# Optimization experiments

Measured on AMD Instinct MI355X. Metric: run time of the kernel, lower is better.

## Reference

```python
import jax, jax.numpy as jnp
import numpy as np

C = 256
NUM_GROUPS = 32
EPS = 1e-5


def group_norm(x, gamma, beta):
    # x: [B, C, H, W]; normalize within each of NUM_GROUPS channel groups
    B, Cc, H, W = x.shape
    xg = x.reshape(B, NUM_GROUPS, Cc // NUM_GROUPS, H, W)
    mean = xg.mean(axis=(2, 3, 4), keepdims=True)
    var = xg.var(axis=(2, 3, 4), keepdims=True)
    xg = (xg - mean) * jax.lax.rsqrt(var + EPS)
    x = xg.reshape(B, Cc, H, W)
    return x * gamma[None, :, None, None] + beta[None, :, None, None]


def conv1x1(x, w, b):
    # w: [C_out, C_in], b: [C_out]; equivalent to nn.Conv2d(k=1)
    return jnp.einsum('oc,bchw->bohw', w, x) + b[None, :, None, None]


def setup_inputs() -> dict:
    key = jax.random.key(0)
    ks = jax.random.split(key, 12)
    B, H, W = 8, 64, 64
    x = jax.random.normal(ks[0], (B, C, H, W), dtype=jnp.float32)
    temb = jax.random.normal(ks[1], (B, 512), dtype=jnp.float32)
    s = 1.0 / np.sqrt(C)  # kaiming-uniform-ish scale for 1x1 conv
    def wmat(k):
        return jax.random.uniform(k, (C, C), dtype=jnp.float32, minval=-s, maxval=s)
    def bvec(k):
        return jax.random.uniform(k, (C,), dtype=jnp.float32, minval=-s, maxval=s)
    return {
        'x': x, 'temb': temb,
        'gn_w': jnp.ones((C,), jnp.float32), 'gn_b': jnp.zeros((C,), jnp.float32),
        'wq': wmat(ks[2]), 'bq': bvec(ks[3]),
        'wk': wmat(ks[4]), 'bk': bvec(ks[5]),
        'wv': wmat(ks[6]), 'bv': bvec(ks[7]),
        'wp': wmat(ks[8]), 'bp': bvec(ks[9]),
    }


def reference(x, temb, gn_w, gn_b, wq, bq, wk, bk, wv, bv, wp, bp):
    B, Cc, H, W = x.shape
    h = group_norm(x, gn_w, gn_b)
    q = conv1x1(h, wq, bq)
    k = conv1x1(h, wk, bk)
    v = conv1x1(h, wv, bv)
    # full self-attention over spatial positions: scores [B, H, W, H, W]
    scale = Cc ** (-0.5)
    w = jnp.einsum('bchw,bcij->bhwij', q, k) * scale
    w = jax.nn.softmax(w.reshape(B, H, W, H * W), axis=-1).reshape(B, H, W, H, W)
    h = jnp.einsum('bhwij,bcij->bchw', w, v)
    h = conv1x1(h, wp, bp)
    return (x + h, temb)
```

## Files before the change

kernel.cpp:

```cpp
#include <hip/hip_runtime.h>
#include <hip/hip_bf16.h>

#define B_ 8
#define C_ 256
#define S_ 4096
#define G_ 32
#define GC_ 8
#define EPS_ 1e-5f

typedef __attribute__((ext_vector_type(4))) float f32x4;
typedef __attribute__((ext_vector_type(8))) short bf16x8;
typedef __attribute__((ext_vector_type(4))) short bf16x4;
typedef __attribute__((ext_vector_type(4))) unsigned int u32x4;
typedef __attribute__((ext_vector_type(2))) unsigned int u32x2;

#define DI __device__ __forceinline__

DI unsigned short f2bf(float f) {
    union { float f; unsigned u; } v; v.f = f;
    unsigned r = v.u + 0x7fffu + ((v.u >> 16) & 1u);
    return (unsigned short)(r >> 16);
}

DI unsigned cvt_pk_bf16(float lo, float hi) {
    unsigned r;
    asm("v_cvt_pk_bf16_f32 %0, %1, %2" : "=v"(r) : "v"(lo), "v"(hi));
    return r;
}

DI unsigned cvt_pk_fp8(float lo, float hi) {
    unsigned r;
    asm("v_cvt_pk_fp8_f32 %0, %1, %2" : "=v"(r) : "v"(lo), "v"(hi));
    return r;
}

DI f32x4 mfma_fp8(u32x2 a, u32x2 b, f32x4 c) {
    union { u32x2 u; long l; } ua, ub;
    ua.u = a; ub.u = b;
    return __builtin_amdgcn_mfma_f32_16x16x32_fp8_fp8(ua.l, ub.l, c, 0, 0, 0);
}

__global__ __launch_bounds__(256) void k_gn_stats(const float* __restrict__ x,
                                                  float* __restrict__ stats) {
    int bg = blockIdx.x;
    const float4* xp = (const float4*)(x + (size_t)bg * (GC_ * S_));
    float s = 0.f, ss = 0.f;
    for (int i = threadIdx.x; i < GC_ * S_ / 4; i += 256) {
        float4 v = xp[i];
        s  += v.x + v.y + v.z + v.w;
        ss += v.x * v.x + v.y * v.y + v.z * v.z + v.w * v.w;
    }
    #pragma unroll
    for (int off = 32; off; off >>= 1) { s += __shfl_down(s, off); ss += __shfl_down(ss, off); }
    __shared__ float rs[4], rss[4];
    int w = threadIdx.x >> 6;
    if ((threadIdx.x & 63) == 0) { rs[w] = s; rss[w] = ss; }
    __syncthreads();
    if (threadIdx.x == 0) {
        float S1 = rs[0] + rs[1] + rs[2] + rs[3];
        float S2 = rss[0] + rss[1] + rss[2] + rss[3];
        float inv = 1.f / (GC_ * S_);
        float mean = S1 * inv;
        float var = S2 * inv - mean * mean;
        stats[bg * 2] = mean;
        stats[bg * 2 + 1] = rsqrtf(var + EPS_);
    }
}

__global__ __launch_bounds__(256) void k_gn_apply(const float* __restrict__ x,
                                                  const float* __restrict__ stats,
                                                  const float* __restrict__ gw,
                                                  const float* __restrict__ gb,
                                                  unsigned short* __restrict__ h) {
    int b = blockIdx.x >> 6;
    int s0 = (blockIdx.x & 63) * 64;
    __shared__ unsigned short tile[64 * 256];
    const float* xb = x + (size_t)b * C_ * S_;
    for (int id = threadIdx.x; id < 256 * 16; id += 256) {
        int c = id >> 4, s4 = id & 15;
        float4 v = *(const float4*)(xb + (size_t)c * S_ + s0 + s4 * 4);
        float mean = stats[(b * G_ + (c >> 3)) * 2];
        float rstd = stats[(b * G_ + (c >> 3)) * 2 + 1];
        float ga = gw[c], be = gb[c];
        float vv[4] = {v.x, v.y, v.z, v.w};
        #pragma unroll
        for (int i = 0; i < 4; i++) {
            int srow = s4 * 4 + i;
            unsigned byte = srow * 512u + c * 2u;
            byte ^= ((srow & 7u) << 4);
            *(unsigned short*)((char*)tile + byte) = f2bf((vv[i] - mean) * rstd * ga + be);
        }
    }
    __syncthreads();
    unsigned short* hb = h + (size_t)b * S_ * C_;
    for (int id = threadIdx.x; id < 2048; id += 256) {
        int srow = id >> 5, ck = id & 31;
        unsigned byte = srow * 512u + ck * 16u;
        byte ^= ((srow & 7u) << 4);
        u32x4 v = *(u32x4*)((char*)tile + byte);
        *(u32x4*)(hb + (size_t)(s0 + srow) * C_ + ck * 8) = v;
    }
}

__global__ __launch_bounds__(256) void k_wcvt(const float* __restrict__ wq, const float* __restrict__ wk,
                                              const float* __restrict__ wv, const float* __restrict__ wp,
                                              unsigned short* __restrict__ wbf) {
    int t = blockIdx.x * 256 + threadIdx.x;
    int mat = t >> 13;
    int idx = (t & 8191) * 8;
    const float* src = mat == 0 ? wq : mat == 1 ? wk : mat == 2 ? wv : wp;
    float4 a = *(const float4*)(src + idx);
    float4 c = *(const float4*)(src + idx + 4);
    unsigned short tmp[8] = {f2bf(a.x), f2bf(a.y), f2bf(a.z), f2bf(a.w),
                             f2bf(c.x), f2bf(c.y), f2bf(c.z), f2bf(c.w)};
    *(u32x4*)(wbf + mat * 65536 + idx) = *(u32x4*)tmp;
}

__global__ __launch_bounds__(256) void k_qkv(const unsigned short* __restrict__ wbf,
                                             const float* __restrict__ bq,
                                             const float* __restrict__ bk,
                                             const float* __restrict__ bv,
                                             const unsigned short* __restrict__ h,
                                             unsigned char* __restrict__ q8,
                                             unsigned char* __restrict__ k8,
                                             unsigned short* __restrict__ v_cs) {
    int mode = blockIdx.x >> 9;
    int inner = blockIdx.x & 511;
    int b = inner & 7;
    int rest = inner >> 3;
    int m0 = (rest & 1) * 128;
    int n0 = (rest >> 1) * 128;
    const unsigned short* W = wbf + mode * 65536;
    const float* bias = mode == 0 ? bq : (mode == 1 ? bk : bv);

    __shared__ unsigned short Alds[128 * 64];
    __shared__ unsigned short Blds[128 * 64];
    int tid = threadIdx.x;
    int lane = tid & 63, wv = tid >> 6;
    int wm = (wv >> 1) * 64, wn = (wv & 1) * 64;
    int lr = lane & 15, lg = lane >> 4;
    f32x4 acc[4][4] = {};
    const unsigned short* Bb = h + (size_t)b * S_ * C_;

    for (int k0 = 0; k0 < 256; k0 += 64) {
        __syncthreads();
        #pragma unroll
        for (int i = 0; i < 4; i++) {
            int id = tid + i * 256;
            int row = id >> 3, ck = id & 7;
            u32x4 v = *(const u32x4*)(W + (size_t)(m0 + row) * C_ + k0 + ck * 8);
            unsigned byte = row * 128u + ck * 16u;
            byte ^= ((row & 7u) << 4);
            *(u32x4*)((char*)Alds + byte) = v;
        }
        #pragma unroll
        for (int i = 0; i < 4; i++) {
            int id = tid + i * 256;
            int row = id >> 3, ck = id & 7;
            u32x4 v = *(const u32x4*)(Bb + (size_t)(n0 + row) * C_ + k0 + ck * 8);
            unsigned byte = row * 128u + ck * 16u;
            byte ^= ((row & 7u) << 4);
            *(u32x4*)((char*)Blds + byte) = v;
        }
        __syncthreads();
        #pragma unroll
        for (int ks = 0; ks < 2; ks++) {
            bf16x8 af[4], bf[4];
            #pragma unroll
            for (int mf = 0; mf < 4; mf++) {
                int m = wm + mf * 16 + lr;
                unsigned byte = m * 128u + ks * 64u + lg * 16u;
                byte ^= ((m & 7u) << 4);
                af[mf] = *(bf16x8*)((char*)Alds + byte);
            }
            #pragma unroll
            for (int nf = 0; nf < 4; nf++) {
                int n = wn + nf * 16 + lr;
                unsigned byte = n * 128u + ks * 64u + lg * 16u;
                byte ^= ((n & 7u) << 4);
                bf[nf] = *(bf16x8*)((char*)Blds + byte);
            }
            #pragma unroll
            for (int mf = 0; mf < 4; mf++)
                #pragma unroll
                for (int nf = 0; nf < 4; nf++)
                    acc[mf][nf] = __builtin_amdgcn_mfma_f32_16x16x32_bf16(af[mf], bf[nf], acc[mf][nf], 0, 0, 0);
        }
    }

    if (mode < 2) {
        unsigned char* ob = (mode == 0 ? q8 : k8) + (size_t)b * S_ * C_;
        #pragma unroll
        for (int mf = 0; mf < 4; mf++)
            #pragma unroll
            for (int nf = 0; nf < 4; nf++) {
                int cbase = m0 + wm + mf * 16 + lg * 4;
                int srow = n0 + wn + nf * 16 + lr;
                float v0 = acc[mf][nf][0] + bias[cbase + 0];
                float v1 = acc[mf][nf][1] + bias[cbase + 1];
                float v2 = acc[mf][nf][2] + bias[cbase + 2];
                float v3 = acc[mf][nf][3] + bias[cbase + 3];
                unsigned lo = cvt_pk_fp8(v0, v1);
                unsigned hi = cvt_pk_fp8(v2, v3);
                *(unsigned*)(ob + (size_t)srow * C_ + cbase) = (lo & 0xffffu) | (hi << 16);
            }
    } else {
        unsigned short* ob = v_cs + (size_t)b * C_ * S_;
        #pragma unroll
        for (int mf = 0; mf < 4; mf++)
            #pragma unroll
            for (int nf = 0; nf < 4; nf++)
                #pragma unroll
                for (int r = 0; r < 4; r++) {
                    int c = m0 + wm + mf * 16 + lg * 4 + r;
                    int s = n0 + wn + nf * 16 + lr;
                    ob[(size_t)c * S_ + s] = f2bf(acc[mf][nf][r] + bias[c]);
                }
    }
}

__global__ __launch_bounds__(256) void k_proj(const unsigned short* __restrict__ wbf,
                                              const float* __restrict__ bias,
                                              const unsigned short* __restrict__ Bm,
                                              float* __restrict__ outf,
                                              const float* __restrict__ xres) {
    int b = blockIdx.x & 7;
    int rest = blockIdx.x >> 3;
    int m0 = (rest & 1) * 128;
    int n0 = (rest >> 1) * 128;
    const unsigned short* W = wbf + 3 * 65536;

    __shared__ unsigned short Alds[128 * 64];
    __shared__ unsigned short Blds[128 * 64];
    int tid = threadIdx.x;
    int lane = tid & 63, wv = tid >> 6;
    int wm = (wv >> 1) * 64, wn = (wv & 1) * 64;
    int lr = lane & 15, lg = lane >> 4;
    f32x4 acc[4][4] = {};
    const unsigned short* Bb = Bm + (size_t)b * S_ * C_;

    for (int k0 = 0; k0 < 256; k0 += 64) {
        __syncthreads();
        #pragma unroll
        for (int i = 0; i < 4; i++) {
            int id = tid + i * 256;
            int row = id >> 3, ck = id & 7;
            u32x4 v = *(const u32x4*)(W + (size_t)(m0 + row) * C_ + k0 + ck * 8);
            unsigned byte = row * 128u + ck * 16u;
            byte ^= ((row & 7u) << 4);
            *(u32x4*)((char*)Alds + byte) = v;
        }
        #pragma unroll
        for (int i = 0; i < 4; i++) {
            int id = tid + i * 256;
            int row = id >> 3, ck = id & 7;
            u32x4 v = *(const u32x4*)(Bb + (size_t)(n0 + row) * C_ + k0 + ck * 8);
            unsigned byte = row * 128u + ck * 16u;
            byte ^= ((row & 7u) << 4);
            *(u32x4*)((char*)Blds + byte) = v;
        }
        __syncthreads();
        #pragma unroll
        for (int ks = 0; ks < 2; ks++) {
            bf16x8 af[4], bf[4];
            #pragma unroll
            for (int mf = 0; mf < 4; mf++) {
                int m = wm + mf * 16 + lr;
                unsigned byte = m * 128u + ks * 64u + lg * 16u;
                byte ^= ((m & 7u) << 4);
                af[mf] = *(bf16x8*)((char*)Alds + byte);
            }
            #pragma unroll
            for (int nf = 0; nf < 4; nf++) {
                int n = wn + nf * 16 + lr;
                unsigned byte = n * 128u + ks * 64u + lg * 16u;
                byte ^= ((n & 7u) << 4);
                bf[nf] = *(bf16x8*)((char*)Blds + byte);
            }
            #pragma unroll
            for (int mf = 0; mf < 4; mf++)
                #pragma unroll
                for (int nf = 0; nf < 4; nf++)
                    acc[mf][nf] = __builtin_amdgcn_mfma_f32_16x16x32_bf16(af[mf], bf[nf], acc[mf][nf], 0, 0, 0);
        }
    }

    const float* xb = xres + (size_t)b * C_ * S_;
    #pragma unroll
    for (int mf = 0; mf < 4; mf++)
        #pragma unroll
        for (int nf = 0; nf < 4; nf++)
            #pragma unroll
            for (int r = 0; r < 4; r++) {
                int c = m0 + wm + mf * 16 + lg * 4 + r;
                int s = n0 + wn + nf * 16 + lr;
                outf[(size_t)b * C_ * S_ + (size_t)c * S_ + s] =
                    acc[mf][nf][r] + bias[c] + xb[(size_t)c * S_ + s];
            }
}

__global__ __launch_bounds__(512, 2) void k_attn(const unsigned char* __restrict__ Q8,
                                                 const unsigned char* __restrict__ K8,
                                                 const unsigned short* __restrict__ V,
                                                 unsigned short* __restrict__ O) {
    int b = blockIdx.x & 7;
    int q0 = (blockIdx.x >> 3) * 128;
    int tid = threadIdx.x, lane = tid & 63, wv = tid >> 6;
    int lr = lane & 15, lg = lane >> 4;
    int qg = wv & 3, kg = wv >> 2;
    int qw = q0 + qg * 32;
    __shared__ unsigned char  Klds8[64 * 256];
    __shared__ unsigned short Vlds[256 * 64];
    __shared__ unsigned short Plds[4][32 * 64];
    __shared__ float mlp[8 * 2 * 16];
    const unsigned char*  Qb = Q8 + (size_t)b * S_ * C_;
    const unsigned char*  Kb = K8 + (size_t)b * S_ * C_;
    const unsigned short* Vb = V + (size_t)b * C_ * S_;

    const float QS = 0.09016844f;

    u32x2 qf8[8][2];
    #pragma unroll
    for (int ks = 0; ks < 8; ks++)
        #pragma unroll
        for (int qf = 0; qf < 2; qf++)
            qf8[ks][qf] = *(const u32x2*)(Qb + (size_t)(qw + qf * 16 + lr) * C_ + ks * 32 + lg * 8);

    unsigned kaddr[2][8];
    #pragma unroll
    for (int kf = 0; kf < 2; kf++) {
        int key = kg * 32 + kf * 16 + lr;
        #pragma unroll
        for (int ks = 0; ks < 8; ks++)
            kaddr[kf][ks] = (unsigned)key * 256u + (((unsigned)(4 * ks + lg + 2 * key) & 31u) << 3);
    }

    f32x4 acc[8][2] = {};
    float lrun[2] = {0.f, 0.f};

    int kr0[2], kc16[2], vc[4], vck[4];
    #pragma unroll
    for (int i = 0; i < 2; i++) {
        int id = tid + i * 512;
        kr0[i] = id >> 4; kc16[i] = id & 15;
    }
    #pragma unroll
    for (int i = 0; i < 4; i++) {
        int id = tid + i * 512;
        vc[i] = id >> 3;  vck[i] = id & 7;
    }
    unsigned kwb[2], vwb[4];
    #pragma unroll
    for (int i = 0; i < 2; i++)
        kwb[i] = kr0[i] * 256u + (((unsigned)(2 * kc16[i] + 2 * kr0[i]) & 31u) << 3);
    #pragma unroll
    for (int i = 0; i < 4; i++)
        vwb[i] = vc[i] * 128u + ((vck[i] * 16u) ^ ((vc[i] & 7u) << 4));

    u32x4 kpre[2], vpre[4];
    #pragma unroll
    for (int i = 0; i < 2; i++)
        kpre[i] = *(const u32x4*)(Kb + (size_t)kr0[i] * C_ + kc16[i] * 16);
    #pragma unroll
    for (int i = 0; i < 4; i++)
        vpre[i] = *(const u32x4*)(Vb + (size_t)vc[i] * S_ + vck[i] * 8);
    #pragma unroll
    for (int i = 0; i < 2; i++)
        *(u32x4*)(Klds8 + kwb[i]) = kpre[i];
    #pragma unroll
    for (int i = 0; i < 4; i++)
        *(u32x4*)((char*)Vlds + vwb[i]) = vpre[i];
    __syncthreads();

    for (int kt = 0; kt < 64; kt++) {
        bool pf = (kt + 1) < 64;
        if (pf) {
            #pragma unroll
            for (int i = 0; i < 2; i++)
                kpre[i] = *(const u32x4*)(Kb + (size_t)((kt + 1) * 64 + kr0[i]) * C_ + kc16[i] * 16);
        }

        f32x4 sc[2][2] = {};
        #pragma unroll
        for (int ks = 0; ks < 8; ks++) {
            u32x2 a0 = *(const u32x2*)(Klds8 + kaddr[0][ks]);
            u32x2 a1 = *(const u32x2*)(Klds8 + kaddr[1][ks]);
            sc[0][0] = mfma_fp8(a0, qf8[ks][0], sc[0][0]);
            sc[0][1] = mfma_fp8(a0, qf8[ks][1], sc[0][1]);
            sc[1][0] = mfma_fp8(a1, qf8[ks][0], sc[1][0]);
            sc[1][1] = mfma_fp8(a1, qf8[ks][1], sc[1][1]);
        }

        #pragma unroll
        for (int qf = 0; qf < 2; qf++)
            #pragma unroll
            for (int kf = 0; kf < 2; kf++) {
                float p0 = __builtin_amdgcn_exp2f(fmaf(sc[kf][qf][0], QS, -16.f));
                float p1 = __builtin_amdgcn_exp2f(fmaf(sc[kf][qf][1], QS, -16.f));
                float p2 = __builtin_amdgcn_exp2f(fmaf(sc[kf][qf][2], QS, -16.f));
                float p3 = __builtin_amdgcn_exp2f(fmaf(sc[kf][qf][3], QS, -16.f));
                lrun[qf] += (p0 + p1) + (p2 + p3);
                u32x2 pk;
                pk[0] = cvt_pk_bf16(p0, p1);
                pk[1] = cvt_pk_bf16(p2, p3);
                int q = qf * 16 + lr;
                unsigned byte = (unsigned)q * 128u + (kg * 32u + kf * 16u + lg * 4u) * 2u;
                byte ^= ((q & 7u) << 4);
                *(u32x2*)((char*)&Plds[qg][0] + byte) = pk;
            }

        if (pf) {
            #pragma unroll
            for (int i = 0; i < 4; i++)
                vpre[i] = *(const u32x4*)(Vb + (size_t)vc[i] * S_ + (kt + 1) * 64 + vck[i] * 8);
        }

        __syncthreads();

        if (pf) {
            #pragma unroll
            for (int i = 0; i < 2; i++)
                *(u32x4*)(Klds8 + kwb[i]) = kpre[i];
        }

        #pragma unroll
        for (int ks2 = 0; ks2 < 2; ks2++) {
            bf16x8 pb[2];
            #pragma unroll
            for (int qf = 0; qf < 2; qf++) {
                int q = qf * 16 + lr;
                unsigned pbyte = (unsigned)q * 128u + ks2 * 64u + lg * 16u;
                pbyte ^= ((q & 7u) << 4);
                pb[qf] = *(const bf16x8*)((char*)&Plds[qg][0] + pbyte);
            }
            #pragma unroll
            for (int cf = 0; cf < 8; cf++) {
                int c = kg * 128 + cf * 16 + lr;
                unsigned byte = c * 128u + ks2 * 64u + lg * 16u;
                byte ^= ((c & 7u) << 4);
                bf16x8 va = *(const bf16x8*)((char*)Vlds + byte);
                #pragma unroll
                for (int qf = 0; qf < 2; qf++)
                    acc[cf][qf] = __builtin_amdgcn_mfma_f32_16x16x32_bf16(va, pb[qf], acc[cf][qf], 0, 0, 0);
            }
        }

        __syncthreads();

        if (pf) {
            #pragma unroll
            for (int i = 0; i < 4; i++)
                *(u32x4*)((char*)Vlds + vwb[i]) = vpre[i];
        }
    }

    float ls[2];
    #pragma unroll
    for (int qf = 0; qf < 2; qf++) {
        float t = lrun[qf];
        t += __shfl_xor(t, 16);
        t += __shfl_xor(t, 32);
        ls[qf] = t;
    }
    if (lg == 0) {
        #pragma unroll
        for (int qf = 0; qf < 2; qf++) mlp[(wv * 2 + qf) * 16 + lr] = ls[qf];
    }
    __syncthreads();
    unsigned short* Ob = O + (size_t)b * S_ * C_;
    #pragma unroll
    for (int qf = 0; qf < 2; qf++) {
        float inv = 1.f / (ls[qf] + mlp[((wv ^ 4) * 2 + qf) * 16 + lr]);
        int srow = qw + qf * 16 + lr;
        #pragma unroll
        for (int cf = 0; cf < 8; cf++) {
            u32x2 pk;
            pk[0] = cvt_pk_bf16(acc[cf][qf][0] * inv, acc[cf][qf][1] * inv);
            pk[1] = cvt_pk_bf16(acc[cf][qf][2] * inv, acc[cf][qf][3] * inv);
            *(u32x2*)(Ob + (size_t)srow * C_ + kg * 128 + cf * 16 + lg * 4) = pk;
        }
    }
}

__global__ __launch_bounds__(256) void k_copy_temb(const float* __restrict__ t, float* __restrict__ o) {
    int i = blockIdx.x * 256 + threadIdx.x;
    if (i < B_ * 512) o[i] = t[i];
}

extern "C" void kernel_launch(void* const* d_in, const int* in_sizes, int n_in,
                              void* d_out, int out_size, void* d_ws, size_t ws_size,
                              hipStream_t stream) {
    (void)in_sizes; (void)n_in; (void)out_size; (void)ws_size;
    const float* x  = (const float*)d_in[0];
    const float* temb = (const float*)d_in[1];
    const float* gw = (const float*)d_in[2];
    const float* gb = (const float*)d_in[3];
    const float* wq = (const float*)d_in[4];
    const float* bq = (const float*)d_in[5];
    const float* wk = (const float*)d_in[6];
    const float* bk = (const float*)d_in[7];
    const float* wv = (const float*)d_in[8];
    const float* bv = (const float*)d_in[9];
    const float* wp = (const float*)d_in[10];
    const float* bp = (const float*)d_in[11];
    float* out = (float*)d_out;

    char* ws = (char*)d_ws;
    const size_t MB = 1024 * 1024;
    unsigned short* h_sc = (unsigned short*)ws;
    unsigned short* v_cs = (unsigned short*)(ws + 16 * MB);
    unsigned char*  q8   = (unsigned char*)(ws + 32 * MB);
    unsigned char*  k8   = (unsigned char*)(ws + 40 * MB);
    float* stats = (float*)(ws + 48 * MB);
    unsigned short* wbf = (unsigned short*)(ws + 48 * MB + 4096);

    k_wcvt<<<128, 256, 0, stream>>>(wq, wk, wv, wp, wbf);
    k_gn_stats<<<B_ * G_, 256, 0, stream>>>(x, stats);
    k_gn_apply<<<B_ * (S_ / 64), 256, 0, stream>>>(x, stats, gw, gb, h_sc);
    k_qkv<<<1536, 256, 0, stream>>>(wbf, bq, bk, bv, h_sc, q8, k8, v_cs);
    k_attn<<<B_ * (S_ / 128), 512, 0, stream>>>(q8, k8, v_cs, h_sc);
    k_proj<<<512, 256, 0, stream>>>(wbf, bp, h_sc, out, x);
    k_copy_temb<<<(B_ * 512 + 255) / 256, 256, 0, stream>>>(temb, out + (size_t)B_ * C_ * S_);
}
```

Baseline: 196.9 us.

## Quantize V and softmax probabilities to fp8 for the PV matmul

Stores V as fp8 instead of bf16 in the QKV kernel and runs the P·V product in the attention kernel with fp8 MFMA, packing probabilities to fp8 in LDS. The exp offset moves from -16 to -2 so the probabilities stay inside fp8 range. LDS tiles switch from XOR-swizzled rows to 72-byte padded rows. The intent is to halve V traffic and LDS footprint and use the faster fp8 MFMA path, at the cost of lower accuracy in the attention output.

```diff
diff --git a/kernel.cpp b/kernel.cpp
--- a/kernel.cpp
+++ b/kernel.cpp
@@ -123,7 +123,7 @@
                                              const unsigned short* __restrict__ h,
                                              unsigned char* __restrict__ q8,
                                              unsigned char* __restrict__ k8,
-                                             unsigned short* __restrict__ v_cs) {
+                                             unsigned char* __restrict__ v8) {
     int mode = blockIdx.x >> 9;
     int inner = blockIdx.x & 511;
     int b = inner & 7;
@@ -205,7 +205,7 @@
                 *(unsigned*)(ob + (size_t)srow * C_ + cbase) = (lo & 0xffffu) | (hi << 16);
             }
     } else {
-        unsigned short* ob = v_cs + (size_t)b * C_ * S_;
+        unsigned char* ob = v8 + (size_t)b * C_ * S_;
         #pragma unroll
         for (int mf = 0; mf < 4; mf++)
             #pragma unroll
@@ -214,7 +214,7 @@
                 for (int r = 0; r < 4; r++) {
                     int c = m0 + wm + mf * 16 + lg * 4 + r;
                     int s = n0 + wn + nf * 16 + lr;
-                    ob[(size_t)c * S_ + s] = f2bf(acc[mf][nf][r] + bias[c]);
+                    ob[(size_t)c * S_ + s] = (unsigned char)(cvt_pk_fp8(acc[mf][nf][r] + bias[c], 0.f) & 0xffu);
                 }
     }
 }
@@ -301,7 +301,7 @@
 
 __global__ __launch_bounds__(512, 2) void k_attn(const unsigned char* __restrict__ Q8,
                                                  const unsigned char* __restrict__ K8,
-                                                 const unsigned short* __restrict__ V,
+                                                 const unsigned char* __restrict__ V8,
                                                  unsigned short* __restrict__ O) {
     int b = blockIdx.x & 7;
     int q0 = (blockIdx.x >> 3) * 128;
@@ -309,13 +309,13 @@
     int lr = lane & 15, lg = lane >> 4;
     int qg = wv & 3, kg = wv >> 2;
     int qw = q0 + qg * 32;
-    __shared__ unsigned char  Klds8[64 * 256];
-    __shared__ unsigned short Vlds[256 * 64];
-    __shared__ unsigned short Plds[4][32 * 64];
+    __shared__ unsigned char Klds8[64 * 256];
+    __shared__ unsigned char Vlds8[256 * 72];
+    __shared__ unsigned char Plds8[4][32 * 72];
     __shared__ float mlp[8 * 2 * 16];
-    const unsigned char*  Qb = Q8 + (size_t)b * S_ * C_;
-    const unsigned char*  Kb = K8 + (size_t)b * S_ * C_;
-    const unsigned short* Vb = V + (size_t)b * C_ * S_;
+    const unsigned char* Qb = Q8 + (size_t)b * S_ * C_;
+    const unsigned char* Kb = K8 + (size_t)b * S_ * C_;
+    const unsigned char* Vb = V8 + (size_t)b * C_ * S_;
 
     const float QS = 0.09016844f;
 
@@ -334,11 +334,14 @@
         for (int ks = 0; ks < 8; ks++)
             kaddr[kf][ks] = (unsigned)key * 256u + (((unsigned)(4 * ks + lg + 2 * key) & 31u) << 3);
     }
+    unsigned vbase[2];
+    vbase[0] = (unsigned)(kg * 128 + lr) * 72u + lg * 8u;
+    vbase[1] = vbase[0] + 32u;
 
     f32x4 acc[8][2] = {};
     float lrun[2] = {0.f, 0.f};
 
-    int kr0[2], kc16[2], vc[4], vck[4];
+    int kr0[2], kc16[2], vc[4], vk8[4];
     #pragma unroll
     for (int i = 0; i < 2; i++) {
         int id = tid + i * 512;
@@ -347,7 +350,7 @@
     #pragma unroll
     for (int i = 0; i < 4; i++) {
         int id = tid + i * 512;
-        vc[i] = id >> 3;  vck[i] = id & 7;
+        vc[i] = id >> 3;  vk8[i] = id & 7;
     }
     unsigned kwb[2], vwb[4];
     #pragma unroll
@@ -355,21 +358,22 @@
         kwb[i] = kr0[i] * 256u + (((unsigned)(2 * kc16[i] + 2 * kr0[i]) & 31u) << 3);
     #pragma unroll
     for (int i = 0; i < 4; i++)
-        vwb[i] = vc[i] * 128u + ((vck[i] * 16u) ^ ((vc[i] & 7u) << 4));
-
-    u32x4 kpre[2], vpre[4];
+        vwb[i] = vc[i] * 72u + vk8[i] * 8u;
+
+    u32x4 kpre[2];
+    u32x2 vpre[4];
     #pragma unroll
     for (int i = 0; i < 2; i++)
         kpre[i] = *(const u32x4*)(Kb + (size_t)kr0[i] * C_ + kc16[i] * 16);
     #pragma unroll
     for (int i = 0; i < 4; i++)
-        vpre[i] = *(const u32x4*)(Vb + (size_t)vc[i] * S_ + vck[i] * 8);
+        vpre[i] = *(const u32x2*)(Vb + (size_t)vc[i] * S_ + vk8[i] * 8);
     #pragma unroll
     for (int i = 0; i < 2; i++)
         *(u32x4*)(Klds8 + kwb[i]) = kpre[i];
     #pragma unroll
     for (int i = 0; i < 4; i++)
-        *(u32x4*)((char*)Vlds + vwb[i]) = vpre[i];
+        *(u32x2*)(Vlds8 + vwb[i]) = vpre[i];
     __syncthreads();
 
     for (int kt = 0; kt < 64; kt++) {
@@ -395,24 +399,20 @@
         for (int qf = 0; qf < 2; qf++)
             #pragma unroll
             for (int kf = 0; kf < 2; kf++) {
-                float p0 = __builtin_amdgcn_exp2f(fmaf(sc[kf][qf][0], QS, -16.f));
-                float p1 = __builtin_amdgcn_exp2f(fmaf(sc[kf][qf][1], QS, -16.f));
-                float p2 = __builtin_amdgcn_exp2f(fmaf(sc[kf][qf][2], QS, -16.f));
-                float p3 = __builtin_amdgcn_exp2f(fmaf(sc[kf][qf][3], QS, -16.f));
+                float p0 = __builtin_amdgcn_exp2f(fmaf(sc[kf][qf][0], QS, -2.f));
+                float p1 = __builtin_amdgcn_exp2f(fmaf(sc[kf][qf][1], QS, -2.f));
+                float p2 = __builtin_amdgcn_exp2f(fmaf(sc[kf][qf][2], QS, -2.f));
+                float p3 = __builtin_amdgcn_exp2f(fmaf(sc[kf][qf][3], QS, -2.f));
                 lrun[qf] += (p0 + p1) + (p2 + p3);
-                u32x2 pk;
-                pk[0] = cvt_pk_bf16(p0, p1);
-                pk[1] = cvt_pk_bf16(p2, p3);
+                unsigned pk = (cvt_pk_fp8(p0, p1) & 0xffffu) | (cvt_pk_fp8(p2, p3) << 16);
                 int q = qf * 16 + lr;
-                unsigned byte = (unsigned)q * 128u + (kg * 32u + kf * 16u + lg * 4u) * 2u;
-                byte ^= ((q & 7u) << 4);
-                *(u32x2*)((char*)&Plds[qg][0] + byte) = pk;
+                *(unsigned*)(&Plds8[qg][0] + (unsigned)q * 72u + kg * 32u + kf * 16u + lg * 4u) = pk;
             }
 
         if (pf) {
             #pragma unroll
             for (int i = 0; i < 4; i++)
-                vpre[i] = *(const u32x4*)(Vb + (size_t)vc[i] * S_ + (kt + 1) * 64 + vck[i] * 8);
+                vpre[i] = *(const u32x2*)(Vb + (size_t)vc[i] * S_ + (kt + 1) * 64 + vk8[i] * 8);
         }
 
         __syncthreads();
@@ -425,23 +425,18 @@
 
         #pragma unroll
         for (int ks2 = 0; ks2 < 2; ks2++) {
-            bf16x8 pb[2];
+            u32x2 pb[2];
             #pragma unroll
             for (int qf = 0; qf < 2; qf++) {
                 int q = qf * 16 + lr;
-                unsigned pbyte = (unsigned)q * 128u + ks2 * 64u + lg * 16u;
-                pbyte ^= ((q & 7u) << 4);
-                pb[qf] = *(const bf16x8*)((char*)&Plds[qg][0] + pbyte);
+                pb[qf] = *(const u32x2*)(&Plds8[qg][0] + (unsigned)q * 72u + ks2 * 32u + lg * 8u);
             }
             #pragma unroll
             for (int cf = 0; cf < 8; cf++) {
-                int c = kg * 128 + cf * 16 + lr;
-                unsigned byte = c * 128u + ks2 * 64u + lg * 16u;
-                byte ^= ((c & 7u) << 4);
-                bf16x8 va = *(const bf16x8*)((char*)Vlds + byte);
+                u32x2 va = *(const u32x2*)(Vlds8 + vbase[ks2] + cf * 1152u);
                 #pragma unroll
                 for (int qf = 0; qf < 2; qf++)
-                    acc[cf][qf] = __builtin_amdgcn_mfma_f32_16x16x32_bf16(va, pb[qf], acc[cf][qf], 0, 0, 0);
+                    acc[cf][qf] = mfma_fp8(va, pb[qf], acc[cf][qf]);
             }
         }
 
@@ -450,7 +445,7 @@
         if (pf) {
             #pragma unroll
             for (int i = 0; i < 4; i++)
-                *(u32x4*)((char*)Vlds + vwb[i]) = vpre[i];
+                *(u32x2*)(Vlds8 + vwb[i]) = vpre[i];
         }
     }
 
@@ -508,17 +503,17 @@
     char* ws = (char*)d_ws;
     const size_t MB = 1024 * 1024;
     unsigned short* h_sc = (unsigned short*)ws;
-    unsigned short* v_cs = (unsigned short*)(ws + 16 * MB);
-    unsigned char*  q8   = (unsigned char*)(ws + 32 * MB);
-    unsigned char*  k8   = (unsigned char*)(ws + 40 * MB);
-    float* stats = (float*)(ws + 48 * MB);
-    unsigned short* wbf = (unsigned short*)(ws + 48 * MB + 4096);
+    unsigned char*  v8   = (unsigned char*)(ws + 16 * MB);
+    unsigned char*  q8   = (unsigned char*)(ws + 24 * MB);
+    unsigned char*  k8   = (unsigned char*)(ws + 32 * MB);
+    float* stats = (float*)(ws + 40 * MB);
+    unsigned short* wbf = (unsigned short*)(ws + 40 * MB + 4096);
 
     k_wcvt<<<128, 256, 0, stream>>>(wq, wk, wv, wp, wbf);
     k_gn_stats<<<B_ * G_, 256, 0, stream>>>(x, stats);
     k_gn_apply<<<B_ * (S_ / 64), 256, 0, stream>>>(x, stats, gw, gb, h_sc);
-    k_qkv<<<1536, 256, 0, stream>>>(wbf, bq, bk, bv, h_sc, q8, k8, v_cs);
-    k_attn<<<B_ * (S_ / 128), 512, 0, stream>>>(q8, k8, v_cs, h_sc);
+    k_qkv<<<1536, 256, 0, stream>>>(wbf, bq, bk, bv, h_sc, q8, k8, v8);
+    k_attn<<<B_ * (S_ / 128), 512, 0, stream>>>(q8, k8, v8, h_sc);
     k_proj<<<512, 256, 0, stream>>>(wbf, bp, h_sc, out, x);
     k_copy_temb<<<(B_ * 512 + 255) / 256, 256, 0, stream>>>(temb, out + (size_t)B_ * C_ * S_);
 }
```

Measured after the change: 193.5 us, median of 3. No clear change (-1.7%).
